# Optimization experiments

Measured on AMD Instinct MI355X. Metric: run time of the kernel, lower is better.

The kernel has to match this reference:

```python
import jax, jax.numpy as jnp
import numpy as np

K = 7          # local window
STRIDE = 1
PAD = 3
M = 8          # channel groups
C = 256
CQ = C // M    # key/query channels (32)
MID = int(0.5 * CQ)  # geometry prior hidden (16)
B, H, W = 4, 56, 56


def _unfold(x, k, stride, pad):
    """torch.nn.Unfold equivalent -> (B, C, L, k, k) with L = ho*wo."""
    b, c, h, w = x.shape
    xp = jnp.pad(x, ((0, 0), (0, 0), (pad, pad), (pad, pad)))
    ho = (h + 2 * pad - k) // stride + 1
    wo = (w + 2 * pad - k) // stride + 1
    cols = jnp.stack(
        [xp[:, :, i:i + stride * ho:stride, j:j + stride * wo:stride]
         for i in range(k) for j in range(k)], axis=-1)  # (B,C,ho,wo,k*k)
    return cols.reshape(b, c, ho * wo, k, k), ho, wo


def _geometry_position(k):
    a = jnp.arange(-(k // 2), k // 2 + 1, dtype=jnp.float32)
    x_pos = jnp.broadcast_to(a[None, :], (k, k))
    b_r = jnp.arange(k // 2, -(k // 2) - 1, -1, dtype=jnp.float32)
    y_pos = jnp.broadcast_to(b_r[:, None], (k, k))
    return jnp.stack([x_pos, y_pos], axis=0)  # (2, k, k)


def setup_inputs() -> dict:
    key = jax.random.key(0)
    ks = jax.random.split(key, 12)
    s = 0.05
    return {
        "x": jax.random.normal(ks[0], (B, C, H, W), jnp.float32),
        "w_k": jax.random.normal(ks[1], (CQ, C), jnp.float32) * s,
        "b_k": jax.random.normal(ks[2], (CQ,), jnp.float32) * s,
        "w_q": jax.random.normal(ks[3], (CQ, C), jnp.float32) * s,
        "b_q": jax.random.normal(ks[4], (CQ,), jnp.float32) * s,
        "w_g1": jax.random.normal(ks[5], (MID, 2), jnp.float32) * s,
        "b_g1": jax.random.normal(ks[6], (MID,), jnp.float32) * s,
        "w_g2": jax.random.normal(ks[7], (CQ, MID), jnp.float32) * s,
        "b_g2": jax.random.normal(ks[8], (CQ,), jnp.float32) * s,
        "w_f": jax.random.normal(ks[9], (C, C), jnp.float32) * s,
        "b_f": jax.random.normal(ks[10], (C,), jnp.float32) * s,
    }


def reference(x, w_k, b_k, w_q, b_q, w_g1, b_g1, w_g2, b_g2, w_f, b_f):
    b = x.shape[0]
    # key/query maps: 1x1 convs C -> CQ
    km = jnp.einsum('bchw,oc->bohw', x, w_k) + b_k[None, :, None, None]
    qm = jnp.einsum('bchw,oc->bohw', x, w_q) + b_q[None, :, None, None]

    km_u, ho, wo = _unfold(km, K, STRIDE, PAD)   # (B,CQ,L,k,k)
    qm_u, _, _ = _unfold(qm, K, STRIDE, PAD)
    center = K * K // 2
    q_center = qm_u.reshape(b, CQ, ho * wo, K * K)[:, :, :, center]  # (B,CQ,L)
    ak = km_u * q_center[:, :, :, None, None]    # (B,CQ,L,k,k)

    # geometry prior: two 1x1 convs on (2,k,k) position grid
    pos = _geometry_position(K)                                   # (2,k,k)
    g1 = jax.nn.relu(jnp.einsum('pij,op->oij', pos, w_g1) + b_g1[:, None, None])
    gpk = jnp.einsum('pij,op->oij', g1, w_g2) + b_g2[:, None, None]  # (CQ,k,k)

    # NOTE: softmax over the LAST k dim only (faithful to original dim=-1)
    ck = jax.nn.softmax(ak + gpk[None, :, None, :, :], axis=-1)   # (B,CQ,L,k,k)

    x_u, _, _ = _unfold(x, K, STRIDE, PAD)                        # (B,C,L,k,k)
    x_u = x_u.reshape(b, M, CQ, ho * wo, K, K)
    # ck broadcasts across the m groups
    pre = jnp.einsum('bclij,bgclij->bgcl', ck, x_u)               # (B,M,CQ,L)
    pre = pre.reshape(b, C, ho, wo)

    out = jnp.einsum('bchw,oc->bohw', pre, w_f) + b_f[None, :, None, None]
    return out
```

## Files before the change

kernel.cpp:

```cpp
#include <hip/hip_runtime.h>
#include <hip/hip_bf16.h>

typedef __hip_bfloat16 bf16;
typedef __attribute__((ext_vector_type(8))) short short8;
typedef __attribute__((ext_vector_type(4))) float floatx4;

#define B_   4
#define C_   256
#define CQ_  32
#define MID_ 16
#define HW_  3136

__device__ __forceinline__ unsigned short f2bf(float f) {
    __hip_bfloat16 h = __float2bfloat16(f);
    return *(unsigned short*)&h;
}

__global__ void __launch_bounds__(256) kq_setup(const float* __restrict__ x,
        const float* __restrict__ w_k, const float* __restrict__ b_k,
        const float* __restrict__ w_q, const float* __restrict__ b_q,
        const float* __restrict__ w_f,
        const float* __restrict__ wg1, const float* __restrict__ bg1,
        const float* __restrict__ wg2, const float* __restrict__ bg2,
        float* __restrict__ km, float* __restrict__ qm,
        short* __restrict__ wfp, float* __restrict__ gpk) {
    int bid = blockIdx.x, t = threadIdx.x;
    if (bid >= 784) {
        if (bid < 800) {
            int base = (bid - 784) * 4096;
            #pragma unroll
            for (int s = 0; s < 16; s++) {
                int j = base + s * 256 + t;
                wfp[j] = (short)f2bf(w_f[(j >> 8) * 256 + (j & 7) * 32 + ((j & 255) >> 3)]);
            }
        } else {
            for (int idx = t; idx < CQ_ * 49; idx += 256) {
                int cq = idx / 49, ij = idx % 49;
                int i = ij / 7, j = ij % 7;
                float xp = (float)(j - 3), yp = (float)(3 - i);
                float acc = bg2[cq];
                #pragma unroll
                for (int o = 0; o < MID_; o++) {
                    float g1 = wg1[o * 2] * xp + wg1[o * 2 + 1] * yp + bg1[o];
                    acc += wg2[cq * MID_ + o] * fmaxf(g1, 0.f);
                }
                gpk[idx] = acc;
            }
        }
        return;
    }
    __shared__ short lt[16 * 264];
    int hw0 = (bid % 196) * 16;
    int b   = bid / 196;

    int pq = t & 3, cb = t >> 2;
    const float* xb = x + (size_t)b * C_ * HW_ + hw0 + pq * 4;
    floatx4 f[4];
    #pragma unroll
    for (int ii = 0; ii < 4; ii++)
        f[ii] = *(const floatx4*)(xb + (size_t)(cb * 4 + ii) * HW_);

    int wave = t >> 6, lane = t & 63, quad = lane >> 4, nl = lane & 15;
    int m0 = wave * 16;
    int row = m0 + nl;
    const float* wsrc = (row < 32) ? (w_k + row * C_) : (w_q + (row - 32) * C_);
    short8 af[8];
    #pragma unroll
    for (int k0 = 0; k0 < 8; k0++) {
        floatx4 wa = *(const floatx4*)(wsrc + k0 * 32 + quad * 8);
        floatx4 wb = *(const floatx4*)(wsrc + k0 * 32 + quad * 8 + 4);
        short8 v;
        #pragma unroll
        for (int u = 0; u < 4; u++) { v[u] = (short)f2bf(wa[u]); v[u + 4] = (short)f2bf(wb[u]); }
        af[k0] = v;
    }

    #pragma unroll
    for (int pr = 0; pr < 2; pr++) {
        int c = cb * 4 + pr * 2;
        int c8 = c >> 3, sub = c & 7;
        #pragma unroll
        for (int u = 0; u < 4; u++) {
            int px = pq * 4 + u;
            unsigned uu = (unsigned)f2bf(f[pr * 2][u]) | ((unsigned)f2bf(f[pr * 2 + 1][u]) << 16);
            *(unsigned*)&lt[px * 264 + ((c8 + pq) & 31) * 8 + sub] = uu;
        }
    }
    __syncthreads();

    floatx4 acc = {0.f, 0.f, 0.f, 0.f};
    int prow = nl * 264, sw = nl >> 2;
    #pragma unroll
    for (int k0 = 0; k0 < 8; k0++) {
        short8 bfr = *(const short8*)&lt[prow + (((k0 * 4 + quad) + sw) & 31) * 8];
        acc = __builtin_amdgcn_mfma_f32_16x16x32_bf16(af[k0], bfr, acc, 0, 0, 0);
    }
    #pragma unroll
    for (int r = 0; r < 4; r++) {
        int ch = m0 + quad * 4 + r;
        bool isK = (ch < 32);
        int c = isK ? ch : ch - 32;
        float bias = isK ? b_k[c] : b_q[c];
        float* dst = (isK ? km : qm) + ((size_t)b * CQ_ + c) * HW_ + hw0 + nl;
        dst[0] = acc[r] + bias;
    }
}

__global__ void __launch_bounds__(448) core_kernel(const float* __restrict__ x,
        const float* __restrict__ km, const float* __restrict__ qm,
        const float* __restrict__ gpk, short* __restrict__ pret) {
    __shared__ float   kms[14 * 62];
    __shared__ floatx4 xs4[2][14 * 62];

    int ht = blockIdx.x, cq = blockIdx.y, b = blockIdx.z;
    int h0 = ht * 8, t = threadIdx.x;

    const float* kmc = km + ((size_t)b * CQ_ + cq) * HW_;
    for (int idx = t; idx < 868; idx += 448) {
        int rr = idx / 62, cc = idx % 62;
        int gh = h0 + rr - 3, gw = cc - 3;
        bool in = ((unsigned)gh < 56u) && ((unsigned)gw < 56u);
        int o = gh * 56 + gw;
        kms[idx] = in ? kmc[o] : 0.f;
        #pragma unroll
        for (int g = 0; g < 2; g++) {
            floatx4 v;
            #pragma unroll
            for (int mm = 0; mm < 4; mm++) {
                const float* xc = x + ((size_t)b * C_ + (g * 4 + mm) * CQ_ + cq) * HW_;
                v[mm] = in ? xc[o] : 0.f;
            }
            xs4[g][idx] = v;
        }
    }
    __syncthreads();

    int r = t / 56, w = t % 56, h = h0 + r;
    float q = qm[((size_t)b * CQ_ + cq) * HW_ + h * 56 + w];
    const float* gp = gpk + cq * 49;

    float ck[49];
    #pragma unroll
    for (int i = 0; i < 7; i++) {
        int base = (r + i) * 62 + w;
        float v[7], s = 0.f;
        #pragma unroll
        for (int j = 0; j < 7; j++) {
            v[j] = __expf(kms[base + j] * q + gp[i * 7 + j]);
            s += v[j];
        }
        float inv = 1.0f / s;
        #pragma unroll
        for (int j = 0; j < 7; j++) ck[i * 7 + j] = v[j] * inv;
    }

    floatx4 a0 = {0.f,0.f,0.f,0.f}, a1 = {0.f,0.f,0.f,0.f};
    #pragma unroll
    for (int i = 0; i < 7; i++) {
        int base = (r + i) * 62 + w;
        #pragma unroll
        for (int j = 0; j < 7; j++) {
            float c = ck[i * 7 + j];
            a0 += c * xs4[0][base + j];
            a1 += c * xs4[1][base + j];
        }
    }

    short8 o8;
    #pragma unroll
    for (int mm = 0; mm < 4; mm++) {
        o8[mm]     = (short)f2bf(a0[mm]);
        o8[mm + 4] = (short)f2bf(a1[mm]);
    }
    __builtin_nontemporal_store(o8, (short8*)(pret + ((size_t)b * HW_ + h * 56 + w) * C_ + cq * 8));
}

__global__ void __launch_bounds__(256) fconv_mfma(const short* __restrict__ pret,
                                                  const short* __restrict__ wfp,
                                                  const float* __restrict__ b_f,
                                                  float* __restrict__ out) {
    int hw0 = blockIdx.x * 64;
    int bm  = blockIdx.y;
    int b   = blockIdx.z;
    int t   = threadIdx.x, wave = t >> 6, lane = t & 63, quad = lane >> 4, nl = lane & 15;
    int m0  = bm * 64 + wave * 16;

    const short* arow = wfp + (m0 + nl) * C_ + quad * 8;
    short8 af[8];
    #pragma unroll
    for (int k0 = 0; k0 < 8; k0++) af[k0] = *(const short8*)(arow + k0 * 32);

    floatx4 acc[4];
    #pragma unroll
    for (int nt = 0; nt < 4; nt++) acc[nt] = (floatx4){0.f,0.f,0.f,0.f};

    const short* pb = pret + ((size_t)b * HW_ + hw0 + nl) * C_ + quad * 8;
    #pragma unroll
    for (int nt = 0; nt < 4; nt++) {
        const short* bp = pb + (size_t)nt * 16 * C_;
        #pragma unroll
        for (int k0 = 0; k0 < 8; k0++)
            acc[nt] = __builtin_amdgcn_mfma_f32_16x16x32_bf16(af[k0], *(const short8*)(bp + k0 * 32),
                                                              acc[nt], 0, 0, 0);
    }

    #pragma unroll
    for (int r = 0; r < 4; r++) {
        int ch = m0 + quad * 4 + r;
        float bias = b_f[ch];
        float* dst = out + ((size_t)b * C_ + ch) * HW_ + hw0 + nl;
        #pragma unroll
        for (int nt = 0; nt < 4; nt++)
            __builtin_nontemporal_store(acc[nt][r] + bias, dst + nt * 16);
    }
}

extern "C" void kernel_launch(void* const* d_in, const int* in_sizes, int n_in,
                              void* d_out, int out_size, void* d_ws, size_t ws_size,
                              hipStream_t stream) {
    const float* x    = (const float*)d_in[0];
    const float* w_k  = (const float*)d_in[1];
    const float* b_k  = (const float*)d_in[2];
    const float* w_q  = (const float*)d_in[3];
    const float* b_q  = (const float*)d_in[4];
    const float* w_g1 = (const float*)d_in[5];
    const float* b_g1 = (const float*)d_in[6];
    const float* w_g2 = (const float*)d_in[7];
    const float* b_g2 = (const float*)d_in[8];
    const float* w_f  = (const float*)d_in[9];
    const float* b_f  = (const float*)d_in[10];
    float* out = (float*)d_out;

    float* ws   = (float*)d_ws;
    float* km   = ws;
    float* qm   = km + (size_t)B_ * CQ_ * HW_;
    float* gpk  = qm + (size_t)B_ * CQ_ * HW_;
    short* wfp  = (short*)(gpk + CQ_ * 49);
    short* pret = wfp + C_ * C_;

    kq_setup<<<dim3(801), 256, 0, stream>>>(x, w_k, b_k, w_q, b_q, w_f,
                                            w_g1, b_g1, w_g2, b_g2, km, qm, wfp, gpk);
    core_kernel<<<dim3(7, CQ_, B_), 448, 0, stream>>>(x, km, qm, gpk, pret);
    fconv_mfma<<<dim3(HW_ / 64, C_ / 64, B_), 256, 0, stream>>>(pret, wfp, b_f, out);
}
```

Measured before the change: 132.3 us.

## Split weight setup from KQ projection, widen KQ tiles, fuse softmax normalization

Weight conversion to bf16 and the geometry prior move into a separate setup kernel. The key/query projection becomes its own MFMA kernel with 32-pixel tiles and 512 threads, and reads pre-converted bf16 weights instead of converting them in every block. The core kernel now folds the per-row softmax normalization into the weighted sum, which removes the 49-entry ck array and multiplies by the reciprocal once per row. The output conv switches from nontemporal to plain stores. The price is one extra kernel launch and a change in how the LDS swizzle is indexed.

```diff
diff --git a/kernel.cpp b/kernel.cpp
--- a/kernel.cpp
+++ b/kernel.cpp
@@ -16,80 +16,79 @@
     return *(unsigned short*)&h;
 }
 
-__global__ void __launch_bounds__(256) kq_setup(const float* __restrict__ x,
-        const float* __restrict__ w_k, const float* __restrict__ b_k,
-        const float* __restrict__ w_q, const float* __restrict__ b_q,
-        const float* __restrict__ w_f,
-        const float* __restrict__ wg1, const float* __restrict__ bg1,
-        const float* __restrict__ wg2, const float* __restrict__ bg2,
-        float* __restrict__ km, float* __restrict__ qm,
-        short* __restrict__ wfp, float* __restrict__ gpk) {
+__global__ void setup_kernel(const float* __restrict__ wk, const float* __restrict__ wq,
+                             const float* __restrict__ wf,
+                             const float* __restrict__ wg1, const float* __restrict__ bg1,
+                             const float* __restrict__ wg2, const float* __restrict__ bg2,
+                             short* __restrict__ wkqb, short* __restrict__ wfp,
+                             float* __restrict__ gpk) {
     int bid = blockIdx.x, t = threadIdx.x;
-    if (bid >= 784) {
-        if (bid < 800) {
-            int base = (bid - 784) * 4096;
-            #pragma unroll
-            for (int s = 0; s < 16; s++) {
-                int j = base + s * 256 + t;
-                wfp[j] = (short)f2bf(w_f[(j >> 8) * 256 + (j & 7) * 32 + ((j & 255) >> 3)]);
-            }
-        } else {
-            for (int idx = t; idx < CQ_ * 49; idx += 256) {
-                int cq = idx / 49, ij = idx % 49;
-                int i = ij / 7, j = ij % 7;
-                float xp = (float)(j - 3), yp = (float)(3 - i);
-                float acc = bg2[cq];
-                #pragma unroll
-                for (int o = 0; o < MID_; o++) {
-                    float g1 = wg1[o * 2] * xp + wg1[o * 2 + 1] * yp + bg1[o];
-                    acc += wg2[cq * MID_ + o] * fmaxf(g1, 0.f);
-                }
-                gpk[idx] = acc;
-            }
-        }
-        return;
-    }
-    __shared__ short lt[16 * 264];
-    int hw0 = (bid % 196) * 16;
-    int b   = bid / 196;
-
-    int pq = t & 3, cb = t >> 2;
+    if (bid < 64) {
+        int i = bid * 256 + t;
+        wkqb[i] = (short)f2bf(i < 8192 ? wk[i] : wq[i - 8192]);
+    } else if (bid < 320) {
+        int j = (bid - 64) * 256 + t;
+        wfp[j] = (short)f2bf(wf[(j >> 8) * 256 + (j & 7) * 32 + ((j & 255) >> 3)]);
+    } else {
+        int idx = (bid - 320) * 256 + t;
+        if (idx >= CQ_ * 49) return;
+        int cq = idx / 49, ij = idx % 49;
+        int i = ij / 7, j = ij % 7;
+        float xp = (float)(j - 3), yp = (float)(3 - i);
+        float acc = bg2[cq];
+        #pragma unroll
+        for (int o = 0; o < MID_; o++) {
+            float g1 = wg1[o * 2] * xp + wg1[o * 2 + 1] * yp + bg1[o];
+            acc += wg2[cq * MID_ + o] * fmaxf(g1, 0.f);
+        }
+        gpk[idx] = acc;
+    }
+}
+
+__global__ void __launch_bounds__(512) kq_mfma(const float* __restrict__ x,
+                                               const short* __restrict__ wkqb,
+                                               const float* __restrict__ b_k,
+                                               const float* __restrict__ b_q,
+                                               float* __restrict__ km, float* __restrict__ qm) {
+    __shared__ short lt[32 * 264];
+    int hw0 = blockIdx.x * 32;
+    int b   = blockIdx.y;
+    int t   = threadIdx.x;
+
+    int pq = t & 7, cb = t >> 3;
     const float* xb = x + (size_t)b * C_ * HW_ + hw0 + pq * 4;
-    floatx4 f[4];
-    #pragma unroll
-    for (int ii = 0; ii < 4; ii++)
-        f[ii] = *(const floatx4*)(xb + (size_t)(cb * 4 + ii) * HW_);
+    floatx4 fa[2], fb[2];
+    #pragma unroll
+    for (int ii = 0; ii < 2; ii++) {
+        int c = ii * 128 + cb * 2;
+        fa[ii] = *(const floatx4*)(xb + (size_t)c * HW_);
+        fb[ii] = *(const floatx4*)(xb + (size_t)(c + 1) * HW_);
+    }
 
     int wave = t >> 6, lane = t & 63, quad = lane >> 4, nl = lane & 15;
-    int m0 = wave * 16;
-    int row = m0 + nl;
-    const float* wsrc = (row < 32) ? (w_k + row * C_) : (w_q + (row - 32) * C_);
+    int m0 = (wave & 3) * 16;
+    int nt = wave >> 2;
+    const short* arow = wkqb + (m0 + nl) * C_ + quad * 8;
     short8 af[8];
     #pragma unroll
-    for (int k0 = 0; k0 < 8; k0++) {
-        floatx4 wa = *(const floatx4*)(wsrc + k0 * 32 + quad * 8);
-        floatx4 wb = *(const floatx4*)(wsrc + k0 * 32 + quad * 8 + 4);
-        short8 v;
-        #pragma unroll
-        for (int u = 0; u < 4; u++) { v[u] = (short)f2bf(wa[u]); v[u + 4] = (short)f2bf(wb[u]); }
-        af[k0] = v;
-    }
-
-    #pragma unroll
-    for (int pr = 0; pr < 2; pr++) {
-        int c = cb * 4 + pr * 2;
+    for (int k0 = 0; k0 < 8; k0++) af[k0] = *(const short8*)(arow + k0 * 32);
+
+    #pragma unroll
+    for (int ii = 0; ii < 2; ii++) {
+        int c = ii * 128 + cb * 2;
         int c8 = c >> 3, sub = c & 7;
         #pragma unroll
         for (int u = 0; u < 4; u++) {
             int px = pq * 4 + u;
-            unsigned uu = (unsigned)f2bf(f[pr * 2][u]) | ((unsigned)f2bf(f[pr * 2 + 1][u]) << 16);
-            *(unsigned*)&lt[px * 264 + ((c8 + pq) & 31) * 8 + sub] = uu;
+            unsigned uu = (unsigned)f2bf(fa[ii][u]) | ((unsigned)f2bf(fb[ii][u]) << 16);
+            *(unsigned*)&lt[px * 264 + ((c8 + (px >> 2)) & 31) * 8 + sub] = uu;
         }
     }
     __syncthreads();
 
+    int px = nt * 16 + nl;
+    int prow = px * 264, sw = px >> 2;
     floatx4 acc = {0.f, 0.f, 0.f, 0.f};
-    int prow = nl * 264, sw = nl >> 2;
     #pragma unroll
     for (int k0 = 0; k0 < 8; k0++) {
         short8 bfr = *(const short8*)&lt[prow + (((k0 * 4 + quad) + sw) & 31) * 8];
@@ -101,7 +100,7 @@
         bool isK = (ch < 32);
         int c = isK ? ch : ch - 32;
         float bias = isK ? b_k[c] : b_q[c];
-        float* dst = (isK ? km : qm) + ((size_t)b * CQ_ + c) * HW_ + hw0 + nl;
+        float* dst = (isK ? km : qm) + ((size_t)b * CQ_ + c) * HW_ + hw0 + px;
         dst[0] = acc[r] + bias;
     }
 }
@@ -139,7 +138,7 @@
     float q = qm[((size_t)b * CQ_ + cq) * HW_ + h * 56 + w];
     const float* gp = gpk + cq * 49;
 
-    float ck[49];
+    floatx4 a0 = {0.f,0.f,0.f,0.f}, a1 = {0.f,0.f,0.f,0.f};
     #pragma unroll
     for (int i = 0; i < 7; i++) {
         int base = (r + i) * 62 + w;
@@ -149,21 +148,16 @@
             v[j] = __expf(kms[base + j] * q + gp[i * 7 + j]);
             s += v[j];
         }
+        floatx4 r0 = {0.f,0.f,0.f,0.f}, r1 = {0.f,0.f,0.f,0.f};
+        #pragma unroll
+        for (int j = 0; j < 7; j++) {
+            float c = v[j];
+            r0 += c * xs4[0][base + j];
+            r1 += c * xs4[1][base + j];
+        }
         float inv = 1.0f / s;
-        #pragma unroll
-        for (int j = 0; j < 7; j++) ck[i * 7 + j] = v[j] * inv;
-    }
-
-    floatx4 a0 = {0.f,0.f,0.f,0.f}, a1 = {0.f,0.f,0.f,0.f};
-    #pragma unroll
-    for (int i = 0; i < 7; i++) {
-        int base = (r + i) * 62 + w;
-        #pragma unroll
-        for (int j = 0; j < 7; j++) {
-            float c = ck[i * 7 + j];
-            a0 += c * xs4[0][base + j];
-            a1 += c * xs4[1][base + j];
-        }
+        a0 += inv * r0;
+        a1 += inv * r1;
     }
 
     short8 o8;
@@ -211,7 +205,7 @@
         float* dst = out + ((size_t)b * C_ + ch) * HW_ + hw0 + nl;
         #pragma unroll
         for (int nt = 0; nt < 4; nt++)
-            __builtin_nontemporal_store(acc[nt][r] + bias, dst + nt * 16);
+            dst[nt * 16] = acc[nt][r] + bias;
     }
 }
 
@@ -235,11 +229,13 @@
     float* km   = ws;
     float* qm   = km + (size_t)B_ * CQ_ * HW_;
     float* gpk  = qm + (size_t)B_ * CQ_ * HW_;
-    short* wfp  = (short*)(gpk + CQ_ * 49);
+    short* wkqb = (short*)(gpk + CQ_ * 49);
+    short* wfp  = wkqb + 64 * C_;
     short* pret = wfp + C_ * C_;
 
-    kq_setup<<<dim3(801), 256, 0, stream>>>(x, w_k, b_k, w_q, b_q, w_f,
-                                            w_g1, b_g1, w_g2, b_g2, km, qm, wfp, gpk);
+    setup_kernel<<<dim3(327), 256, 0, stream>>>(w_k, w_q, w_f, w_g1, b_g1, w_g2, b_g2,
+                                                wkqb, wfp, gpk);
+    kq_mfma<<<dim3(HW_ / 32, B_), 512, 0, stream>>>(x, wkqb, b_k, b_q, km, qm);
     core_kernel<<<dim3(7, CQ_, B_), 448, 0, stream>>>(x, km, qm, gpk, pret);
     fconv_mfma<<<dim3(HW_ / 64, C_ / 64, B_), 256, 0, stream>>>(pret, wfp, b_f, out);
 }
```

Measured after the change: 130.9 us. About the same (-1.1%).
